# Performance work log

Measured on AMD Instinct MI355X. Metric: run time of the kernel, lower is better.

The kernel has to match this reference:

```python
import jax, jax.numpy as jnp
import numpy as np

VOX_X, VOX_Y, VOX_Z = 256, 256, 20   # ceil((pc_range[3:]-pc_range[:3]) / 0.4)
OUT_H, OUT_W, OUT_Z = 200, 200, 16   # hard-coded F.interpolate target in forward
C = 80                               # out_channels; sparse feat dim must match for concat
N_PTS = 200000
BS = 1
EPS = 1e-5


def _lin_interp(x, axis, out_size):
    """1D linear interp along `axis`, matching torch align_corners=False."""
    in_size = x.shape[axis]
    pos = (jnp.arange(out_size, dtype=jnp.float32) + 0.5) * (in_size / out_size) - 0.5
    pos = jnp.clip(pos, 0.0, in_size - 1)
    i0 = jnp.floor(pos).astype(jnp.int32)
    i1 = jnp.minimum(i0 + 1, in_size - 1)
    w = pos - i0.astype(jnp.float32)
    x0 = jnp.take(x, i0, axis=axis)
    x1 = jnp.take(x, i1, axis=axis)
    wshape = [1] * x.ndim
    wshape[axis] = out_size
    w = w.reshape(wshape)
    return x0 * (1.0 - w) + x1 * w


def setup_inputs() -> dict:
    key = jax.random.key(0)
    ks = jax.random.split(key, 8)
    bev_feats = jax.random.normal(ks[0], (BS, C, OUT_H, OUT_W, OUT_Z), dtype=jnp.float32)
    # coords: [batch_idx, x, y, z] with per-column valid ranges
    cb = jax.random.randint(ks[1], (N_PTS, 1), 0, BS, dtype=jnp.int32)
    cx = jax.random.randint(ks[2], (N_PTS, 1), 0, VOX_X, dtype=jnp.int32)
    cy = jax.random.randint(ks[3], (N_PTS, 1), 0, VOX_Y, dtype=jnp.int32)
    cz = jax.random.randint(ks[4], (N_PTS, 1), 0, VOX_Z, dtype=jnp.int32)
    coords = jnp.concatenate([cb, cx, cy, cz], axis=1)
    feats = jax.random.normal(ks[5], (N_PTS, C), dtype=jnp.float32)
    w_conv = jax.random.normal(ks[6], (C, 2 * C), dtype=jnp.float32) * (1.0 / np.sqrt(2 * C))
    b_conv = jnp.zeros((C,), dtype=jnp.float32)
    return {
        "bev_feats": bev_feats, "coords": coords, "feats": feats,
        "w_conv": w_conv, "b_conv": b_conv,
        "bn_gamma": jnp.ones((C,), jnp.float32), "bn_beta": jnp.zeros((C,), jnp.float32),
        "bn_mean": jnp.zeros((C,), jnp.float32), "bn_var": jnp.ones((C,), jnp.float32),
    }


def reference(bev_feats, coords, feats, w_conv, b_conv, bn_gamma, bn_beta, bn_mean, bn_var):
    bs = bev_feats.shape[0]
    voxel = jnp.zeros((bs, VOX_X, VOX_Y, VOX_Z, C), dtype=jnp.float32)
    voxel = voxel.at[coords[:, 0], coords[:, 1], coords[:, 2], coords[:, 3]].set(feats)
    # permute(0,4,2,1,3): (bs, X, Y, Z, C) -> (bs, C, Y, X, Z)
    prior = jnp.transpose(voxel, (0, 4, 2, 1, 3))
    # trilinear interpolate (256,256,20) -> (200,200,16), align_corners=False (separable)
    prior = _lin_interp(prior, 2, OUT_H)
    prior = _lin_interp(prior, 3, OUT_W)
    prior = _lin_interp(prior, 4, OUT_Z)
    # concat on channels -> 1x1x1 conv3d -> BN (eval stats) -> residual -> ReLU
    x = jnp.concatenate([bev_feats, prior], axis=1)  # (bs, 2C, H, W, Z)
    y = jnp.einsum('bchwz,oc->bohwz', x, w_conv) + b_conv[None, :, None, None, None]
    inv = bn_gamma * jax.lax.rsqrt(bn_var + EPS)
    y = y * inv[None, :, None, None, None] + (bn_beta - bn_mean * inv)[None, :, None, None, None]
    return jax.nn.relu(y + bev_feats)
```

## Files before the change

kernel.cpp:

```cpp
#include <hip/hip_runtime.h>
#include <hip/hip_bf16.h>

#define VXX 256
#define VYY 256
#define VZZ 20
#define NC  80
#define OH  200
#define OW  200
#define OZ  16
#define SPATIAL (OH*OW*OZ)
#define NVOX (VXX*VYY*VZZ)
#define EPSV 1e-5f
#define NS 64
#define RS 168
#define NWG (SPATIAL/NS)
#define X_FOOT 6
#define NCELL (2*X_FOOT*VZZ)
#define SLOTS 48
#define STR32 41

typedef float  f32x4 __attribute__((ext_vector_type(4)));
typedef short  s16x8 __attribute__((ext_vector_type(8)));

__device__ __forceinline__ ushort f2bf(float f) {
    uint u = __builtin_bit_cast(uint, f);
    u += 0x7FFFu + ((u >> 16) & 1u);
    return (ushort)(u >> 16);
}

__device__ __forceinline__ void bar_lgkm() {
    asm volatile("s_waitcnt lgkmcnt(0)" ::: "memory");
    __builtin_amdgcn_s_barrier();
    asm volatile("" ::: "memory");
}

__global__ void scatter_k(const int* __restrict__ coords, int npts,
                          int* __restrict__ winner) {
    int i = blockIdx.x * 256 + threadIdx.x;
    if (i >= npts) return;
    int b = coords[i*4+0];
    int x = coords[i*4+1];
    int y = coords[i*4+2];
    int z = coords[i*4+3];
    int vi = ((b*VXX + x)*VYY + y)*VZZ + z;
    atomicMax(&winner[vi], i);
}

__global__ void setup_k(const float* __restrict__ wconv,
                        const float* __restrict__ bconv,
                        const float* __restrict__ gamma,
                        const float* __restrict__ beta,
                        const float* __restrict__ mean,
                        const float* __restrict__ var,
                        int4* __restrict__ winner4,
                        ushort* __restrict__ wfrag,
                        float2* __restrict__ bnss) {
    const int b = blockIdx.x, tid = threadIdx.x;
    if (b < 1280) {
        winner4[b*256 + tid] = make_int4(-1, -1, -1, -1);
    } else if (b < 1330) {
        int idx = (b - 1280)*256 + tid;
        int f   = idx >> 9;
        int rem = idx & 511;
        int l   = rem >> 3;
        int j   = rem & 7;
        int mt  = f / 5;
        int ks  = f - mt*5;
        int o   = mt*16 + (l & 15);
        int c   = ks*32 + (l >> 4)*8 + j;
        wfrag[idx] = f2bf(wconv[o*160 + c]);
    } else if (tid < NC) {
        float inv = gamma[tid] * rsqrtf(var[tid] + EPSV);
        bnss[tid] = make_float2(inv, bconv[tid]*inv + beta[tid] - mean[tid]*inv);
    }
}

__launch_bounds__(256, 5)
__global__ void fused_k(const float* __restrict__ bev,
                        const float* __restrict__ feats,
                        const int*  __restrict__ winner,
                        const ushort* __restrict__ wfrag,
                        const float2* __restrict__ bnss,
                        float* __restrict__ out) {
    __shared__ __align__(16) ushort x_lds[NS * RS];
    __shared__ uint   rows_lds[SLOTS*STR32];
    __shared__ int    idx_lds[NCELL];
    __shared__ int    slot_pi[SLOTS];
    __shared__ int    wavecnt[4];

    const int tid   = threadIdx.x;
    const int bid   = blockIdx.x;
    const int swzb  = (bid & 7) * (NWG/8) + (bid >> 3);
    const int sbase = swzb * NS;
    const int sl    = tid & 63;
    const int quarter = tid >> 6;
    const int wv    = quarter, lane = sl;

    const int h  = sbase / (OW * OZ);
    const int w0 = (sbase >> 4) % OW;
    float posy = (h + 0.5f) * ((float)VYY/(float)OH) - 0.5f;
    posy = fminf(fmaxf(posy, 0.f), (float)(VYY-1));
    const int   y0 = (int)posy;
    const int   y1 = min(y0+1, VYY-1);
    const float fy = posy - (float)y0;
    float posx0 = (w0 + 0.5f) * ((float)VXX/(float)OW) - 0.5f;
    posx0 = fminf(fmaxf(posx0, 0.f), (float)(VXX-1));
    const int xmin = (int)posx0;

    int pi = -1;
    if (tid < NCELL) {
        int fz  = tid % VZZ;
        int fx  = (tid / VZZ) % X_FOOT;
        int fyc = tid / (VZZ * X_FOOT);
        int xx  = min(xmin + fx, VXX-1);
        int yy  = fyc ? y1 : y0;
        pi = winner[(xx*VYY + yy)*VZZ + fz];
    }
    __builtin_amdgcn_sched_barrier(0);

    const int S = sbase + sl;
    float bvv[20];
    #pragma unroll
    for (int j = 0; j < 20; ++j)
        bvv[j] = bev[(quarter*20 + j)*SPATIAL + S];
    __builtin_amdgcn_sched_barrier(0);

    unsigned long long bm = __ballot(pi >= 0);
    if (lane == 0) wavecnt[wv] = __popcll(bm);
    bar_lgkm();
    int base = 0, nstot = 0;
    #pragma unroll
    for (int w2 = 0; w2 < 4; ++w2) {
        int c2 = wavecnt[w2];
        if (w2 < wv) base += c2;
        nstot += c2;
    }
    if (tid < NCELL) {
        int v = -1;
        if (pi >= 0) {
            int slot = base + __popcll(bm & ((1ull << lane) - 1ull));
            if (slot < SLOTS) { slot_pi[slot] = pi; v = slot; }
            else v = -(pi + 2);
        }
        idx_lds[tid] = v;
    }
    bar_lgkm();
    const int nst = min(nstot, SLOTS);

    const float4* feats4 = (const float4*)feats;
    const int myslot = tid >> 2, part = tid & 3;
    const bool rowact = (myslot < nst);
    float4 rbuf[5];
    if (rowact) {
        const float4* p = feats4 + slot_pi[myslot]*20 + part*5;
        #pragma unroll
        for (int q = 0; q < 5; ++q) rbuf[q] = p[q];
    }

    #pragma unroll
    for (int j5 = 0; j5 < 5; ++j5) {
        ushort4 pk = make_ushort4(f2bf(bvv[j5*4+0]), f2bf(bvv[j5*4+1]),
                                  f2bf(bvv[j5*4+2]), f2bf(bvv[j5*4+3]));
        *(ushort4*)&x_lds[sl*RS + quarter*20 + j5*4] = pk;
    }

    if (rowact) {
        uint* dst = &rows_lds[myslot*STR32 + part*10];
        #pragma unroll
        for (int q = 0; q < 5; ++q) {
            dst[2*q]   = (uint)f2bf(rbuf[q].x) | ((uint)f2bf(rbuf[q].y) << 16);
            dst[2*q+1] = (uint)f2bf(rbuf[q].z) | ((uint)f2bf(rbuf[q].w) << 16);
        }
    }
    bar_lgkm();

    {
        const int z = sl & 15;
        const int w = w0 + (sl >> 4);
        float posx = (w + 0.5f) * ((float)VXX/(float)OW) - 0.5f;
        posx = fminf(fmaxf(posx, 0.f), (float)(VXX-1));
        int x0 = (int)posx; int x1 = min(x0+1, VXX-1);
        float fxw = posx - (float)x0;
        float posz = (z + 0.5f) * ((float)VZZ/(float)OZ) - 0.5f;
        posz = fminf(fmaxf(posz, 0.f), (float)(VZZ-1));
        int z0 = (int)posz; int z1 = min(z0+1, VZZ-1);
        float fzw = posz - (float)z0;
        const int fx0 = x0 - xmin, fx1 = x1 - xmin;

        float acc20[20];
        #pragma unroll
        for (int j = 0; j < 20; ++j) acc20[j] = 0.f;

        #pragma unroll
        for (int k = 0; k < 8; ++k) {
            int kz = k & 1, kx = (k>>1)&1, ky = k>>2;
            int cell = (ky*X_FOOT + (kx ? fx1 : fx0))*VZZ + (kz ? z1 : z0);
            int v = idx_lds[cell];
            if (v == -1) continue;
            float wtk = (ky?fy:1.f-fy) * (kx?fxw:1.f-fxw) * (kz?fzw:1.f-fzw);
            if (v >= 0) {
                const uint* r = &rows_lds[v*STR32 + quarter*10];
                #pragma unroll
                for (int qq = 0; qq < 10; ++qq) {
                    uint u = r[qq];
                    float lo = __builtin_bit_cast(float, u << 16);
                    float hi = __builtin_bit_cast(float, u & 0xffff0000u);
                    acc20[2*qq]   += wtk * lo;
                    acc20[2*qq+1] += wtk * hi;
                }
            } else {
                const float4* p = feats4 + (-v - 2)*20 + quarter*5;
                #pragma unroll
                for (int q = 0; q < 5; ++q) {
                    float4 f = p[q];
                    acc20[4*q]   += wtk*f.x; acc20[4*q+1] += wtk*f.y;
                    acc20[4*q+2] += wtk*f.z; acc20[4*q+3] += wtk*f.w;
                }
            }
        }

        #pragma unroll
        for (int q = 0; q < 5; ++q) {
            ushort4 pk = make_ushort4(f2bf(acc20[4*q]),   f2bf(acc20[4*q+1]),
                                      f2bf(acc20[4*q+2]), f2bf(acc20[4*q+3]));
            *(ushort4*)&x_lds[sl*RS + 80 + quarter*20 + q*4] = pk;
        }
    }
    bar_lgkm();

    const int lrow = lane & 15, lgrp = lane >> 4;

    f32x4 acc[5];
    #pragma unroll
    for (int mt = 0; mt < 5; ++mt) acc[mt] = (f32x4){0.f, 0.f, 0.f, 0.f};

    const int srow = (wv*16 + lrow) * RS;

    #pragma unroll
    for (int ks = 0; ks < 5; ++ks) {
        s16x8 b = *(const s16x8*)&x_lds[srow + ks*32 + lgrp*8];
        #pragma unroll
        for (int mt = 0; mt < 5; ++mt) {
            s16x8 a = *(const s16x8*)&wfrag[((mt*5 + ks)*64 + lane)*8];
            acc[mt] = __builtin_amdgcn_mfma_f32_16x16x32_bf16(a, b, acc[mt], 0, 0, 0);
        }
    }

    const int slocal = wv*16 + lrow;
    const int sglob  = sbase + slocal;
    #pragma unroll
    for (int mt = 0; mt < 5; ++mt) {
        ushort4 rr = *(const ushort4*)&x_lds[slocal*RS + mt*16 + lgrp*4];
        const ushort rrv[4] = {rr.x, rr.y, rr.z, rr.w};
        #pragma unroll
        for (int r = 0; r < 4; ++r) {
            int o = mt*16 + lgrp*4 + r;
            float2 ss = bnss[o];
            float resid = __builtin_bit_cast(float, (uint)rrv[r] << 16);
            float v = acc[mt][r]*ss.x + ss.y + resid;
            out[o*SPATIAL + sglob] = fmaxf(v, 0.f);
        }
    }
}

extern "C" void kernel_launch(void* const* d_in, const int* in_sizes, int n_in,
                              void* d_out, int out_size, void* d_ws, size_t ws_size,
                              hipStream_t stream) {
    const float* bev    = (const float*)d_in[0];
    const int*   coords = (const int*)  d_in[1];
    const float* feats  = (const float*)d_in[2];
    const float* wconv  = (const float*)d_in[3];
    const float* bconv  = (const float*)d_in[4];
    const float* gamma  = (const float*)d_in[5];
    const float* beta   = (const float*)d_in[6];
    const float* mean   = (const float*)d_in[7];
    const float* var    = (const float*)d_in[8];
    float*       out    = (float*)d_out;

    int*    winner = (int*)d_ws;
    ushort* wfrag  = (ushort*)((char*)d_ws + (size_t)NVOX*4);
    float2* bnss   = (float2*)((char*)d_ws + (size_t)NVOX*4 + 25600);
    int npts = in_sizes[1] / 4;

    hipLaunchKernelGGL(setup_k, dim3(1331), dim3(256), 0, stream,
                       wconv, bconv, gamma, beta, mean, var,
                       (int4*)winner, wfrag, bnss);
    hipLaunchKernelGGL(scatter_k, dim3((npts + 255)/256), dim3(256), 0, stream,
                       coords, npts, winner);
    hipLaunchKernelGGL(fused_k, dim3(NWG), dim3(256), 0, stream,
                       bev, feats, winner, wfrag, bnss, out);
}
```

Measured before the change: 153.2 us.

## Compute trilinear interpolation as a sparse weight-matrix MFMA over gathered voxel rows

Replaces the per-thread scalar trilinear accumulation from LDS rows with a small matrix product. A per-block weight matrix P (64 samples × 64 slots) and transposed feature rows Rt (80 channels × 64 slots) are built in LDS, then two bf16 MFMAs per channel tile produce the interpolated prior. Overflow voxels beyond the slot capacity are still added in a scalar fixup path. LDS usage grows and launch bounds drop from 5 to 3 blocks per CU, which lowers occupancy. Rounding the weights to bf16 adds some precision loss.

```diff
diff --git a/kernel.cpp b/kernel.cpp
--- a/kernel.cpp
+++ b/kernel.cpp
@@ -17,7 +17,7 @@
 #define X_FOOT 6
 #define NCELL (2*X_FOOT*VZZ)
 #define SLOTS 48
-#define STR32 41
+#define PSTR 72
 
 typedef float  f32x4 __attribute__((ext_vector_type(4)));
 typedef short  s16x8 __attribute__((ext_vector_type(8)));
@@ -75,7 +75,7 @@
     }
 }
 
-__launch_bounds__(256, 5)
+__launch_bounds__(256, 3)
 __global__ void fused_k(const float* __restrict__ bev,
                         const float* __restrict__ feats,
                         const int*  __restrict__ winner,
@@ -83,7 +83,8 @@
                         const float2* __restrict__ bnss,
                         float* __restrict__ out) {
     __shared__ __align__(16) ushort x_lds[NS * RS];
-    __shared__ uint   rows_lds[SLOTS*STR32];
+    __shared__ __align__(16) ushort P_lds[NS * PSTR];
+    __shared__ __align__(16) ushort Rt_lds[NC * PSTR];
     __shared__ int    idx_lds[NCELL];
     __shared__ int    slot_pi[SLOTS];
     __shared__ int    wavecnt[4];
@@ -107,6 +108,20 @@
     posx0 = fminf(fmaxf(posx0, 0.f), (float)(VXX-1));
     const int xmin = (int)posx0;
 
+    const int zq = sl & 15;
+    const int wq = w0 + (sl >> 4);
+    float posx = (wq + 0.5f) * ((float)VXX/(float)OW) - 0.5f;
+    posx = fminf(fmaxf(posx, 0.f), (float)(VXX-1));
+    const int   x0 = (int)posx;
+    const int   x1 = min(x0+1, VXX-1);
+    const float fxw = posx - (float)x0;
+    float posz = (zq + 0.5f) * ((float)VZZ/(float)OZ) - 0.5f;
+    posz = fminf(fmaxf(posz, 0.f), (float)(VZZ-1));
+    const int   z0 = (int)posz;
+    const int   z1 = min(z0+1, VZZ-1);
+    const float fzw = posz - (float)z0;
+    const int fx0 = x0 - xmin, fx1 = x1 - xmin;
+
     int pi = -1;
     if (tid < NCELL) {
         int fz  = tid % VZZ;
@@ -125,6 +140,12 @@
         bvv[j] = bev[(quarter*20 + j)*SPATIAL + S];
     __builtin_amdgcn_sched_barrier(0);
 
+    {
+        uint* pz = (uint*)P_lds;
+        #pragma unroll
+        for (int i = 0; i < 9; ++i) pz[tid + i*256] = 0;
+    }
+
     unsigned long long bm = __ballot(pi >= 0);
     if (lane == 0) wavecnt[wv] = __popcll(bm);
     bar_lgkm();
@@ -157,6 +178,23 @@
         for (int q = 0; q < 5; ++q) rbuf[q] = p[q];
     }
 
+    {
+        const int ky = quarter >> 1, kx = quarter & 1;
+        const float ywp = ky ? fy : 1.f - fy;
+        const bool xdup = (fx1 == fx0);
+        if (!(xdup && kx)) {
+            const int   xf = kx ? fx1 : fx0;
+            const float xw = xdup ? 1.f : (kx ? fxw : 1.f - fxw);
+            #pragma unroll
+            for (int kz = 0; kz < 2; ++kz) {
+                int cell = (ky*X_FOOT + xf)*VZZ + (kz ? z1 : z0);
+                int v = idx_lds[cell];
+                if (v >= 0)
+                    P_lds[sl*PSTR + v] = f2bf(ywp * xw * (kz ? fzw : 1.f - fzw));
+            }
+        }
+    }
+
     #pragma unroll
     for (int j5 = 0; j5 < 5; ++j5) {
         ushort4 pk = make_ushort4(f2bf(bvv[j5*4+0]), f2bf(bvv[j5*4+1]),
@@ -164,71 +202,80 @@
         *(ushort4*)&x_lds[sl*RS + quarter*20 + j5*4] = pk;
     }
 
-    if (rowact) {
-        uint* dst = &rows_lds[myslot*STR32 + part*10];
+    {
+        ushort vals[20];
         #pragma unroll
         for (int q = 0; q < 5; ++q) {
-            dst[2*q]   = (uint)f2bf(rbuf[q].x) | ((uint)f2bf(rbuf[q].y) << 16);
-            dst[2*q+1] = (uint)f2bf(rbuf[q].z) | ((uint)f2bf(rbuf[q].w) << 16);
-        }
+            vals[4*q+0] = rowact ? f2bf(rbuf[q].x) : (ushort)0;
+            vals[4*q+1] = rowact ? f2bf(rbuf[q].y) : (ushort)0;
+            vals[4*q+2] = rowact ? f2bf(rbuf[q].z) : (ushort)0;
+            vals[4*q+3] = rowact ? f2bf(rbuf[q].w) : (ushort)0;
+        }
+        #pragma unroll
+        for (int e = 0; e < 20; ++e)
+            Rt_lds[(part*20 + e)*PSTR + myslot] = vals[e];
     }
     bar_lgkm();
 
+    const int lrow = lane & 15, lgrp = lane >> 4;
     {
-        const int z = sl & 15;
-        const int w = w0 + (sl >> 4);
-        float posx = (w + 0.5f) * ((float)VXX/(float)OW) - 0.5f;
-        posx = fminf(fmaxf(posx, 0.f), (float)(VXX-1));
-        int x0 = (int)posx; int x1 = min(x0+1, VXX-1);
-        float fxw = posx - (float)x0;
-        float posz = (z + 0.5f) * ((float)VZZ/(float)OZ) - 0.5f;
-        posz = fminf(fmaxf(posz, 0.f), (float)(VZZ-1));
-        int z0 = (int)posz; int z1 = min(z0+1, VZZ-1);
-        float fzw = posz - (float)z0;
-        const int fx0 = x0 - xmin, fx1 = x1 - xmin;
-
-        float acc20[20];
-        #pragma unroll
-        for (int j = 0; j < 20; ++j) acc20[j] = 0.f;
-
+        const int prow = (wv*16 + lrow)*PSTR;
+        s16x8 p0 = *(const s16x8*)&P_lds[prow +      lgrp*8];
+        s16x8 p1 = *(const s16x8*)&P_lds[prow + 32 + lgrp*8];
+        #pragma unroll
+        for (int mt = 0; mt < 5; ++mt) {
+            const int arow = (mt*16 + lrow)*PSTR;
+            s16x8 a0 = *(const s16x8*)&Rt_lds[arow +      lgrp*8];
+            s16x8 a1 = *(const s16x8*)&Rt_lds[arow + 32 + lgrp*8];
+            f32x4 pa = (f32x4){0.f, 0.f, 0.f, 0.f};
+            pa = __builtin_amdgcn_mfma_f32_16x16x32_bf16(a0, p0, pa, 0, 0, 0);
+            pa = __builtin_amdgcn_mfma_f32_16x16x32_bf16(a1, p1, pa, 0, 0, 0);
+            ushort4 pk = make_ushort4(f2bf(pa[0]), f2bf(pa[1]),
+                                      f2bf(pa[2]), f2bf(pa[3]));
+            *(ushort4*)&x_lds[(wv*16 + lrow)*RS + 80 + mt*16 + lgrp*4] = pk;
+        }
+    }
+
+    if (nstot > SLOTS) {
+        bar_lgkm();
+        float add20[20];
+        #pragma unroll
+        for (int j = 0; j < 20; ++j) add20[j] = 0.f;
+        bool any = false;
         #pragma unroll
         for (int k = 0; k < 8; ++k) {
             int kz = k & 1, kx = (k>>1)&1, ky = k>>2;
             int cell = (ky*X_FOOT + (kx ? fx1 : fx0))*VZZ + (kz ? z1 : z0);
             int v = idx_lds[cell];
-            if (v == -1) continue;
-            float wtk = (ky?fy:1.f-fy) * (kx?fxw:1.f-fxw) * (kz?fzw:1.f-fzw);
-            if (v >= 0) {
-                const uint* r = &rows_lds[v*STR32 + quarter*10];
-                #pragma unroll
-                for (int qq = 0; qq < 10; ++qq) {
-                    uint u = r[qq];
-                    float lo = __builtin_bit_cast(float, u << 16);
-                    float hi = __builtin_bit_cast(float, u & 0xffff0000u);
-                    acc20[2*qq]   += wtk * lo;
-                    acc20[2*qq+1] += wtk * hi;
-                }
-            } else {
+            if (v < -1) {
+                any = true;
+                float wtk = (ky?fy:1.f-fy) * (kx?fxw:1.f-fxw) * (kz?fzw:1.f-fzw);
                 const float4* p = feats4 + (-v - 2)*20 + quarter*5;
                 #pragma unroll
                 for (int q = 0; q < 5; ++q) {
                     float4 f = p[q];
-                    acc20[4*q]   += wtk*f.x; acc20[4*q+1] += wtk*f.y;
-                    acc20[4*q+2] += wtk*f.z; acc20[4*q+3] += wtk*f.w;
+                    add20[4*q]   += wtk*f.x; add20[4*q+1] += wtk*f.y;
+                    add20[4*q+2] += wtk*f.z; add20[4*q+3] += wtk*f.w;
                 }
             }
         }
-
-        #pragma unroll
-        for (int q = 0; q < 5; ++q) {
-            ushort4 pk = make_ushort4(f2bf(acc20[4*q]),   f2bf(acc20[4*q+1]),
-                                      f2bf(acc20[4*q+2]), f2bf(acc20[4*q+3]));
-            *(ushort4*)&x_lds[sl*RS + 80 + quarter*20 + q*4] = pk;
+        if (any) {
+            #pragma unroll
+            for (int q = 0; q < 5; ++q) {
+                ushort* dst = &x_lds[sl*RS + 80 + quarter*20 + q*4];
+                ushort4 old = *(ushort4*)dst;
+                const ushort ov[4] = {old.x, old.y, old.z, old.w};
+                ushort nv[4];
+                #pragma unroll
+                for (int e = 0; e < 4; ++e) {
+                    float f = __builtin_bit_cast(float, (uint)ov[e] << 16) + add20[4*q+e];
+                    nv[e] = f2bf(f);
+                }
+                *(ushort4*)dst = make_ushort4(nv[0], nv[1], nv[2], nv[3]);
+            }
         }
     }
     bar_lgkm();
-
-    const int lrow = lane & 15, lgrp = lane >> 4;
 
     f32x4 acc[5];
     #pragma unroll
```

After: 149.5 us (median of 2 runs). 2.5% less time.
